# Kernel optimization log

Hardware: AMD Instinct MI355X
Metric: run time of the kernel (lower is better)

The kernel has to match this reference:

```python
import jax, jax.numpy as jnp
import numpy as np

B = 8
NF = 64
COUNTS = [1200, 1400, 1500, 1536, 1600, 1700, 1800, 1552]  # ragged per-batch point counts
ND = 12288  # total decoder points (= sum(COUNTS))
NE = 12288  # total encoder points
LQ = 1800   # max per-batch count (padding length)
EPS = 1e-4  # scn BatchNormalization eps


def _build_geometry():
    """Random sparse 3D voxel coords per batch on a 64^3 grid; parent cells (coord//2)
    are unique by construction so the stride-2 downsample keeps one point per cell
    and Nkv == Nd with the same per-batch ordering (matches the module's slicing)."""
    rng = np.random.default_rng(0)
    coords = []
    for b, c in enumerate(COUNTS):
        cells = rng.choice(32 * 32 * 32, size=c, replace=False)
        x, y, z = cells // 1024, (cells // 32) % 32, cells % 32
        off = rng.integers(0, 2, size=(c, 3))
        pts = np.stack([x, y, z], 1) * 2 + off
        coords.append(np.concatenate([np.full((c, 1), b), pts], 1))
    coords = np.concatenate(coords, 0)  # [ND, 4] = (batch, x, y, z)
    lut = {tuple(r): i for i, r in enumerate(coords)}
    offs = np.array([[dx, dy, dz] for dx in (-1, 0, 1) for dy in (-1, 0, 1) for dz in (-1, 0, 1)])
    nbr = np.full((ND, 27), -1, np.int32)  # 3^3 submanifold rulebook
    for i, r in enumerate(coords):
        for k, o in enumerate(offs):
            j = lut.get((r[0], r[1] + o[0], r[2] + o[1], r[3] + o[2]))
            if j is not None:
                nbr[i, k] = j
    kv_nbr = np.full((ND, 8), -1, np.int32)  # stride-2 2^3 conv rulebook (1 child per cell)
    off_id = (coords[:, 1] % 2) * 4 + (coords[:, 2] % 2) * 2 + (coords[:, 3] % 2)
    kv_nbr[np.arange(ND), off_id] = np.arange(ND)
    pad_idx = np.full((B, LQ), -1, np.int32)
    unpad_idx = np.zeros(ND, np.int32)
    s = 0
    for b, c in enumerate(COUNTS):
        pad_idx[b, :c] = np.arange(s, s + c)
        unpad_idx[s:s + c] = b * LQ + np.arange(c)
        s += c
    return nbr, kv_nbr, pad_idx, unpad_idx


def setup_inputs() -> dict:
    nbr, kv_nbr, pad_idx, unpad_idx = _build_geometry()
    key = jax.random.key(0)
    ks = jax.random.split(key, 16)
    w = lambda k, i, o: jax.random.normal(k, (i, o), jnp.float32) / np.sqrt(i)
    w3 = lambda k, t, i, o: jax.random.normal(k, (t, i, o), jnp.float32) / np.sqrt(t * i)
    return {
        "x_decoder": jax.random.normal(ks[0], (ND, NF), jnp.float32),
        "x_encoder": jax.random.normal(ks[1], (NE, NF), jnp.float32),
        "Wp1": w(ks[2], NF, NF), "Wq": w(ks[3], NF, NF), "Wk": w(ks[4], NF, NF),
        "Wv": w(ks[5], NF, NF), "Wt": w(ks[6], NF, NF), "Wq1": w(ks[7], NF, NF),
        "Wk1": w(ks[8], NF, NF), "Wv1": w(ks[9], NF, NF),
        "Wdown": w3(ks[10], 8, NF, NF),
        "W3t": w3(ks[11], 27, NF, NF), "W3a": w3(ks[12], 27, NF, NF), "W3b": w3(ks[13], 27, NF, NF),
        "bn_gamma": jnp.ones((6, NF), jnp.float32),
        "bn_beta": jnp.zeros((6, NF), jnp.float32),
        "nbr": jnp.asarray(nbr), "kv_nbr": jnp.asarray(kv_nbr),
        "pad_idx": jnp.asarray(pad_idx), "unpad_idx": jnp.asarray(unpad_idx),
    }


def _bn(x, g, b):  # training-mode scn.BatchNormalization over all active points
    m = jnp.mean(x, 0)
    v = jnp.mean(jnp.square(x - m), 0)
    return (x - m) * jax.lax.rsqrt(v + EPS) * g + b


def _gconv(f, idx, W):  # rulebook sparse conv: idx [N,K] (-1 = missing), W [K,F,O]
    mask = (idx >= 0).astype(f.dtype)[..., None]
    g = f[jnp.clip(idx, 0)] * mask  # [N, K, F]
    return jnp.einsum('nkf,kfo->no', g, W)


def _pad(f, pad_idx):  # flat [N,F] -> padded [B,L,F] + validity mask [B,L]
    m = pad_idx >= 0
    return f[jnp.clip(pad_idx, 0)] * m[..., None].astype(f.dtype), m


def reference(x_decoder, x_encoder, Wp1, Wq, Wk, Wv, Wt, Wq1, Wk1, Wv1,
              Wdown, W3t, W3a, W3b, bn_gamma, bn_beta,
              nbr, kv_nbr, pad_idx, unpad_idx):
    xd = x_decoder @ Wp1                      # p1 (1x1 submanifold conv)
    q = xd @ Wq
    ke = x_encoder @ Wk
    ve = x_encoder @ Wv
    # Stage-1 cross attention. The torch loop slices queries per batch but always
    # uses the FULL encoder K/V (dk = features.T), so it equals one global attention.
    attn = jax.nn.softmax(q @ ke.T, axis=-1)  # [ND, NE], no 1/sqrt(d) scaling in source
    xr = (attn @ ve) @ Wt                     # trans_conv (1x1)
    xd = xd + _bn(xr, bn_gamma[0], bn_beta[0])  # after_norm residual add

    q1 = xd @ Wq1
    kv = _bn(_gconv(q1, kv_nbr, Wdown), bn_gamma[1], bn_beta[1])  # stride-2 conv + BN
    k1 = kv @ Wk1
    v1 = kv @ Wv1
    # Stage-2 ragged per-batch self attention (Nkv == Nd by construction).
    qp, _ = _pad(q1, pad_idx)                 # [B, LQ, NF]
    kp, mkv = _pad(k1, pad_idx)
    vp, _ = _pad(v1, pad_idx)
    s2 = jnp.einsum('blf,bmf->blm', qp, kp)
    s2 = jnp.where(mkv[:, None, :], s2, jnp.float32(-1e30))
    o = jnp.einsum('blm,bmf->blf', jax.nn.softmax(s2, axis=-1), vp)
    xr2 = o.reshape(B * LQ, NF)[unpad_idx]    # back to flat ragged layout [ND, NF]
    xr2 = _gconv(xr2, nbr, W3t)               # trans_conv1 (3^3 submanifold conv)
    xd = xd + _bn(xr2, bn_gamma[2], bn_beta[2])  # after_norm1 residual add

    # res block: BNReLU -> conv3 -> BNReLU -> conv3, add identity, BNReLU
    z = _gconv(jax.nn.relu(_bn(xd, bn_gamma[3], bn_beta[3])), nbr, W3a)
    z = _gconv(jax.nn.relu(_bn(z, bn_gamma[4], bn_beta[4])), nbr, W3b)
    return jax.nn.relu(_bn(xd + z, bn_gamma[5], bn_beta[5]))
```

## Files before the change

### kernel.cpp

```cpp
#include <hip/hip_runtime.h>

#define NPTS 12288
#define LQPAD 1800
#define LPAD2 1856
#define EPSBN 1e-4f

typedef _Float16 half8 __attribute__((ext_vector_type(8)));
typedef _Float16 half4 __attribute__((ext_vector_type(4)));
typedef float floatx4 __attribute__((ext_vector_type(4)));

__global__ __launch_bounds__(256) void wprod(const float* __restrict__ Wp1, const float* __restrict__ Wq,
                                             float* __restrict__ Wpq) {
    __shared__ float A[4096], Bs[4096];
    int t = threadIdx.x;
    for (int i = t; i < 4096; i += 256) {
        A[i] = Wp1[i];
        Bs[i] = Wq[i];
    }
    __syncthreads();
    for (int o = 0; o < 16; o++) {
        int idx = o * 256 + t;
        int i = idx >> 6, j = idx & 63;
        float s = 0.f;
#pragma unroll
        for (int k = 0; k < 64; k++) s += A[i * 64 + k] * Bs[k * 64 + j];
        Wpq[idx] = s;
    }
}

__global__ __launch_bounds__(256) void pack_all(const float* Wp1, const float* Wpq, const float* Wk,
                                                const float* Wv, const float* Wt_, const float* Wq1,
                                                const float* Wk1, const float* Wv1, const float* Wdown,
                                                const float* W3t, const float* W3a, const float* W3b,
                                                _Float16* __restrict__ Wf) {
    int g = blockIdx.x;
    const float* src;
    if (g == 0) src = Wp1;
    else if (g == 1) src = Wpq;
    else if (g == 2) src = Wk;
    else if (g == 3) src = Wv;
    else if (g == 4) src = Wt_;
    else if (g == 5) src = Wq1;
    else if (g == 6) src = Wk1;
    else if (g == 7) src = Wv1;
    else if (g < 16) src = Wdown + (size_t)(g - 8) * 4096;
    else if (g < 43) src = W3t + (size_t)(g - 16) * 4096;
    else if (g < 70) src = W3a + (size_t)(g - 43) * 4096;
    else src = W3b + (size_t)(g - 70) * 4096;
    int t = threadIdx.x;
    int lane = t & 63, fg = t >> 6;
    int quad = lane >> 4, qi = lane & 15;
#pragma unroll
    for (int u = 0; u < 2; u++) {
        int frag = fg * 2 + u;
        int s = frag >> 2, ct = frag & 3;
        half8 v;
#pragma unroll
        for (int j = 0; j < 8; j++) v[j] = (_Float16)src[(s * 32 + quad * 8 + j) * 64 + ct * 16 + qi];
        *(half8*)(Wf + (size_t)g * 4096 + frag * 512 + lane * 8) = v;
    }
}

__device__ inline void load_split8(const float* p, half8& hi, half8& lo) {
    float4 a = *(const float4*)p;
    float4 b = *(const float4*)(p + 4);
    float v[8] = {a.x, a.y, a.z, a.w, b.x, b.y, b.z, b.w};
#pragma unroll
    for (int j = 0; j < 8; j++) {
        _Float16 h = (_Float16)v[j];
        hi[j] = h;
        lo[j] = (_Float16)(v[j] - (float)h);
    }
}

__global__ __launch_bounds__(256) void gemm_head(const float* __restrict__ xdec, const float* __restrict__ xenc,
                                                 const _Float16* __restrict__ Wf, float* __restrict__ xd,
                                                 _Float16* __restrict__ Qh, _Float16* __restrict__ Ql,
                                                 _Float16* __restrict__ Kh, _Float16* __restrict__ Vt) {
    int z = blockIdx.y;
    const float* A = (z < 2) ? xdec : xenc;
    const _Float16* Bf = Wf + (size_t)z * 4096;
    int t = threadIdx.x;
    int lane = t & 63, wv = t >> 6;
    int quad = lane >> 4, qi = lane & 15;
    int row0w = blockIdx.x * 64 + wv * 16;
    half8 ah[2], al[2];
#pragma unroll
    for (int s = 0; s < 2; s++) load_split8(A + (size_t)(row0w + qi) * 64 + s * 32 + quad * 8, ah[s], al[s]);
    floatx4 C[4];
#pragma unroll
    for (int ct = 0; ct < 4; ct++) C[ct] = floatx4{0.f, 0.f, 0.f, 0.f};
#pragma unroll
    for (int ct = 0; ct < 4; ct++)
#pragma unroll
        for (int s = 0; s < 2; s++) {
            half8 b = *(const half8*)(Bf + (s * 4 + ct) * 512 + lane * 8);
            C[ct] = __builtin_amdgcn_mfma_f32_16x16x32_f16(ah[s], b, C[ct], 0, 0, 0);
            C[ct] = __builtin_amdgcn_mfma_f32_16x16x32_f16(al[s], b, C[ct], 0, 0, 0);
        }
    int orow = row0w + quad * 4;
    if (z == 0) {
#pragma unroll
        for (int ct = 0; ct < 4; ct++)
#pragma unroll
            for (int r = 0; r < 4; r++) xd[(size_t)(orow + r) * 64 + ct * 16 + qi] = C[ct][r];
    } else if (z == 1) {
#pragma unroll
        for (int ct = 0; ct < 4; ct++)
#pragma unroll
            for (int r = 0; r < 4; r++) {
                float v = C[ct][r];
                _Float16 h = (_Float16)v;
                Qh[(size_t)(orow + r) * 64 + ct * 16 + qi] = h;
                Ql[(size_t)(orow + r) * 64 + ct * 16 + qi] = (_Float16)(v - (float)h);
            }
    } else if (z == 2) {
#pragma unroll
        for (int ct = 0; ct < 4; ct++)
#pragma unroll
            for (int r = 0; r < 4; r++) Kh[(size_t)(orow + r) * 64 + ct * 16 + qi] = (_Float16)C[ct][r];
    } else {
#pragma unroll
        for (int ct = 0; ct < 4; ct++) {
            half4 o;
#pragma unroll
            for (int r = 0; r < 4; r++) o[r] = (_Float16)C[ct][r];
            *(half4*)(Vt + (size_t)(ct * 16 + qi) * NPTS + orow) = o;
        }
    }
}

__global__ __launch_bounds__(256) void gemm_split(const float* __restrict__ A, const _Float16* __restrict__ Bf,
                                                  _Float16* __restrict__ Oh, _Float16* __restrict__ Ol) {
    int t = threadIdx.x;
    int lane = t & 63, wv = t >> 6;
    int quad = lane >> 4, qi = lane & 15;
    int row0w = blockIdx.x * 64 + wv * 16;
    half8 ah[2], al[2];
#pragma unroll
    for (int s = 0; s < 2; s++) load_split8(A + (size_t)(row0w + qi) * 64 + s * 32 + quad * 8, ah[s], al[s]);
    floatx4 C[4];
#pragma unroll
    for (int ct = 0; ct < 4; ct++) C[ct] = floatx4{0.f, 0.f, 0.f, 0.f};
#pragma unroll
    for (int ct = 0; ct < 4; ct++)
#pragma unroll
        for (int s = 0; s < 2; s++) {
            half8 b = *(const half8*)(Bf + (s * 4 + ct) * 512 + lane * 8);
            C[ct] = __builtin_amdgcn_mfma_f32_16x16x32_f16(ah[s], b, C[ct], 0, 0, 0);
            C[ct] = __builtin_amdgcn_mfma_f32_16x16x32_f16(al[s], b, C[ct], 0, 0, 0);
        }
    int orow = row0w + quad * 4;
#pragma unroll
    for (int ct = 0; ct < 4; ct++)
#pragma unroll
        for (int r = 0; r < 4; r++) {
            float v = C[ct][r];
            _Float16 h = (_Float16)v;
            Oh[(size_t)(orow + r) * 64 + ct * 16 + qi] = h;
            Ol[(size_t)(orow + r) * 64 + ct * 16 + qi] = (_Float16)(v - (float)h);
        }
}

__global__ __launch_bounds__(256) void gemm_kv1(const float* __restrict__ kv, const _Float16* __restrict__ Wfk,
                                                const _Float16* __restrict__ Wfv,
                                                const float* __restrict__ stats, const float* __restrict__ gamma,
                                                const float* __restrict__ beta, const int* __restrict__ unpad,
                                                _Float16* __restrict__ Kh1, _Float16* __restrict__ Vt2) {
    int y = blockIdx.y;
    int t = threadIdx.x;
    int lane = t & 63, wv = t >> 6;
    int quad = lane >> 4, qi = lane & 15;
    int row0w = blockIdx.x * 64 + wv * 16;
    const float inv_n = 1.f / (float)NPTS;
    half8 ah[2], al[2];
#pragma unroll
    for (int s = 0; s < 2; s++) {
        const float* p = kv + (size_t)(row0w + qi) * 64 + s * 32 + quad * 8;
        float4 a = *(const float4*)p;
        float4 b2 = *(const float4*)(p + 4);
        float v[8] = {a.x, a.y, a.z, a.w, b2.x, b2.y, b2.z, b2.w};
#pragma unroll
        for (int j = 0; j < 8; j++) {
            int f = s * 32 + quad * 8 + j;
            float mean = stats[f] * inv_n;
            float var = stats[64 + f] * inv_n - mean * mean;
            float val = (v[j] - mean) * rsqrtf(var + EPSBN) * gamma[f] + beta[f];
            _Float16 h = (_Float16)val;
            ah[s][j] = h;
            al[s][j] = (_Float16)(val - (float)h);
        }
    }
    const _Float16* Bf = y ? Wfv : Wfk;
    floatx4 C[4];
#pragma unroll
    for (int ct = 0; ct < 4; ct++) C[ct] = floatx4{0.f, 0.f, 0.f, 0.f};
#pragma unroll
    for (int ct = 0; ct < 4; ct++)
#pragma unroll
        for (int s = 0; s < 2; s++) {
            half8 b = *(const half8*)(Bf + (s * 4 + ct) * 512 + lane * 8);
            C[ct] = __builtin_amdgcn_mfma_f32_16x16x32_f16(ah[s], b, C[ct], 0, 0, 0);
            C[ct] = __builtin_amdgcn_mfma_f32_16x16x32_f16(al[s], b, C[ct], 0, 0, 0);
        }
    int orow = row0w + quad * 4;
    if (y == 0) {
#pragma unroll
        for (int ct = 0; ct < 4; ct++)
#pragma unroll
            for (int r = 0; r < 4; r++) Kh1[(size_t)(orow + r) * 64 + ct * 16 + qi] = (_Float16)C[ct][r];
    } else {
        int u0 = unpad[orow], u3 = unpad[orow + 3];
        int b0 = u0 / 1800, b3 = u3 / 1800;
        if (u3 == u0 + 3 && b0 == b3) {
            int p0 = u0 - b0 * 1800;
#pragma unroll
            for (int ct = 0; ct < 4; ct++) {
                half4 o;
#pragma unroll
                for (int r = 0; r < 4; r++) o[r] = (_Float16)C[ct][r];
                *(half4*)(Vt2 + ((size_t)b0 * 64 + ct * 16 + qi) * LPAD2 + p0) = o;
            }
        } else {
#pragma unroll
            for (int r = 0; r < 4; r++) {
                int u = unpad[orow + r];
                int b = u / 1800, p = u - b * 1800;
#pragma unroll
                for (int ct = 0; ct < 4; ct++)
                    Vt2[((size_t)b * 64 + ct * 16 + qi) * LPAD2 + p] = (_Float16)C[ct][r];
            }
        }
    }
}

__global__ __launch_bounds__(256) void gconv_mfma(const _Float16* __restrict__ Xh,
                                                  const int* __restrict__ idx,
                                                  const _Float16* __restrict__ Wf,
                                                  float* __restrict__ OUT, int nk,
                                                  const float* Xadd, float* stats_out) {
    __shared__ float s_sum[64], s_ss[64];
    int t = threadIdx.x;
    int lane = t & 63, wv = t >> 6;
    int quad = lane >> 4, qi = lane & 15;
    int row0 = blockIdx.x * 64 + wv * 16;
    if (stats_out) {
        if (t < 64) {
            s_sum[t] = 0.f;
            s_ss[t] = 0.f;
        }
        __syncthreads();
    }
    floatx4 Oacc[4];
#pragma unroll
    for (int ct = 0; ct < 4; ct++) Oacc[ct] = floatx4{0.f, 0.f, 0.f, 0.f};
    const int* ip = idx + (size_t)(row0 + qi) * nk;
    for (int k = 0; k < nk; k++) {
        int j = ip[k];
        half8 a0 = half8{0, 0, 0, 0, 0, 0, 0, 0};
        half8 a1 = half8{0, 0, 0, 0, 0, 0, 0, 0};
        if (j >= 0) {
            a0 = *(const half8*)(Xh + (size_t)j * 64 + quad * 8);
            a1 = *(const half8*)(Xh + (size_t)j * 64 + 32 + quad * 8);
        }
        const _Float16* wk = Wf + (size_t)k * 4096;
#pragma unroll
        for (int ct = 0; ct < 4; ct++) {
            half8 b0 = *(const half8*)(wk + ct * 512 + lane * 8);
            half8 b1 = *(const half8*)(wk + (4 + ct) * 512 + lane * 8);
            Oacc[ct] = __builtin_amdgcn_mfma_f32_16x16x32_f16(a0, b0, Oacc[ct], 0, 0, 0);
            Oacc[ct] = __builtin_amdgcn_mfma_f32_16x16x32_f16(a1, b1, Oacc[ct], 0, 0, 0);
        }
    }
    int orow = row0 + quad * 4;
#pragma unroll
    for (int ct = 0; ct < 4; ct++)
#pragma unroll
        for (int r = 0; r < 4; r++) OUT[(size_t)(orow + r) * 64 + ct * 16 + qi] = Oacc[ct][r];
    if (stats_out) {
#pragma unroll
        for (int ct = 0; ct < 4; ct++) {
            int f = ct * 16 + qi;
            float ps = 0.f, pss = 0.f;
#pragma unroll
            for (int r = 0; r < 4; r++) {
                float v = Oacc[ct][r];
                if (Xadd) v += Xadd[(size_t)(orow + r) * 64 + f];
                ps += v;
                pss += v * v;
            }
            atomicAdd(&s_sum[f], ps);
            atomicAdd(&s_ss[f], pss);
        }
        __syncthreads();
        if (t < 64) {
            atomicAdd(&stats_out[t], s_sum[t]);
            atomicAdd(&stats_out[64 + t], s_ss[t]);
        }
    }
}

__global__ __launch_bounds__(256) void bn_apply(const float* __restrict__ X, const float* X2,
                                                const float* R, float* OUT, _Float16* OUT16,
                                                const float* __restrict__ stats,
                                                const float* __restrict__ gamma,
                                                const float* __restrict__ beta,
                                                float* stats_out, int n, int do_relu) {
    __shared__ float sh[2][4][64];
    int t = threadIdx.x;
    int f = t & 63, g = t >> 6;
    float inv_n = 1.f / (float)n;
    float mean = stats[f] * inv_n;
    float var = stats[64 + f] * inv_n - mean * mean;
    float rstd = rsqrtf(var + EPSBN);
    float ga = gamma[f], be = beta[f];
    float s = 0.f, ss = 0.f;
    for (int r = blockIdx.x * 4 + g; r < n; r += gridDim.x * 4) {
        size_t i = (size_t)r * 64 + f;
        float v = X[i];
        if (X2) v += X2[i];
        v = (v - mean) * rstd * ga + be;
        if (R) v += R[i];
        if (do_relu) v = fmaxf(v, 0.f);
        if (OUT) OUT[i] = v;
        if (OUT16) OUT16[i] = (_Float16)v;
        s += v;
        ss += v * v;
    }
    if (stats_out) {
        sh[0][g][f] = s;
        sh[1][g][f] = ss;
        __syncthreads();
        if (g == 0) {
            s = sh[0][0][f] + sh[0][1][f] + sh[0][2][f] + sh[0][3][f];
            ss = sh[1][0][f] + sh[1][1][f] + sh[1][2][f] + sh[1][3][f];
            atomicAdd(&stats_out[f], s);
            atomicAdd(&stats_out[64 + f], ss);
        }
    }
}

__global__ __launch_bounds__(256) void count_valid(const int* __restrict__ pad_idx, int* __restrict__ counts) {
    int b = blockIdx.x;
    int t = threadIdx.x;
    int s = 0;
    for (int i = t; i < LQPAD; i += 256) s += (pad_idx[b * LQPAD + i] >= 0) ? 1 : 0;
    for (int off = 32; off > 0; off >>= 1) s += __shfl_xor(s, off);
    if ((t & 63) == 0) atomicAdd(&counts[b], s);
}

__global__ __launch_bounds__(256, 3) void flash1_mfma(const _Float16* __restrict__ Qh,
                                                      const _Float16* __restrict__ Ql,
                                                      const _Float16* __restrict__ Kh,
                                                      const _Float16* __restrict__ Vt,
                                                      _Float16* __restrict__ Op,
                                                      float* __restrict__ Ms,
                                                      float* __restrict__ Ls) {
    __shared__ __align__(16) _Float16 KsF[8 * 512];
    __shared__ __align__(16) _Float16 VsF[8 * 512];
    __shared__ __align__(16) _Float16 PTF[4][2 * 1024];
    int t = threadIdx.x;
    int lane = t & 63, wv = t >> 6;
    int quad = lane >> 4, qi = lane & 15;
    int qb = blockIdx.x, sp = blockIdx.y;
    int q0w = qb * 128 + wv * 32;

    half8 qh[2][2], ql[2][2];
#pragma unroll
    for (int sub = 0; sub < 2; sub++)
#pragma unroll
        for (int s = 0; s < 2; s++) {
            int qrow = q0w + sub * 16 + qi;
            qh[sub][s] = *(const half8*)(Qh + (size_t)qrow * 64 + s * 32 + quad * 8);
            ql[sub][s] = *(const half8*)(Ql + (size_t)qrow * 64 + s * 32 + quad * 8);
        }
    floatx4 Oacc[2][4];
#pragma unroll
    for (int sub = 0; sub < 2; sub++)
#pragma unroll
        for (int ft = 0; ft < 4; ft++) Oacc[sub][ft] = floatx4{0.f, 0.f, 0.f, 0.f};
    float m_i[2] = {-1e30f, -1e30f}, l_i[2] = {0.f, 0.f};

    for (int it = 0; it < 24; it++) {
        int k0 = sp * 1536 + it * 64;
        __syncthreads();
#pragma unroll
        for (int u = 0; u < 4; u++) {
            int frag = wv + 4 * u;
            if (frag < 8) {
                int kt = frag >> 1, s = frag & 1;
                int key = k0 + kt * 16 + qi;
                *(half8*)(KsF + frag * 512 + lane * 8) =
                    *(const half8*)(Kh + (size_t)key * 64 + s * 32 + quad * 8);
            } else {
                int fr = frag - 8;
                int ft = fr >> 1, s = fr & 1;
                int f = ft * 16 + qi;
                *(half8*)(VsF + fr * 512 + lane * 8) =
                    *(const half8*)(Vt + (size_t)f * NPTS + k0 + s * 32 + quad * 8);
            }
        }
        __syncthreads();
        half8 ka[4][2];
#pragma unroll
        for (int kt = 0; kt < 4; kt++)
#pragma unroll
            for (int s = 0; s < 2; s++) ka[kt][s] = *(const half8*)(KsF + (kt * 2 + s) * 512 + lane * 8);
        floatx4 st[2][4];
#pragma unroll
        for (int sub = 0; sub < 2; sub++)
#pragma unroll
            for (int kt = 0; kt < 4; kt++) {
                floatx4 acc = floatx4{0.f, 0.f, 0.f, 0.f};
#pragma unroll
                for (int s = 0; s < 2; s++) {
                    acc = __builtin_amdgcn_mfma_f32_16x16x32_f16(ka[kt][s], qh[sub][s], acc, 0, 0, 0);
                    acc = __builtin_amdgcn_mfma_f32_16x16x32_f16(ka[kt][s], ql[sub][s], acc, 0, 0, 0);
                }
                st[sub][kt] = acc;
            }
#pragma unroll
        for (int sub = 0; sub < 2; sub++) {
            float mloc = -1e30f;
#pragma unroll
            for (int kt = 0; kt < 4; kt++)
#pragma unroll
                for (int r = 0; r < 4; r++) mloc = fmaxf(mloc, st[sub][kt][r]);
            mloc = fmaxf(mloc, __shfl_xor(mloc, 16));
            mloc = fmaxf(mloc, __shfl_xor(mloc, 32));
            float m_new = fmaxf(m_i[sub], mloc);
            float alpha = __expf(m_i[sub] - m_new);
            float ps = 0.f;
#pragma unroll
            for (int kt = 0; kt < 4; kt++) {
                half4 pk;
#pragma unroll
                for (int r = 0; r < 4; r++) {
                    float p = __expf(st[sub][kt][r] - m_new);
                    ps += p;
                    pk[r] = (_Float16)p;
                }
                int s = kt >> 1;
                int qd2 = (kt & 1) * 2 + (quad >> 1);
                *(half4*)(&PTF[wv][sub * 1024 + (s * 64 + qd2 * 16 + qi) * 8 + (quad & 1) * 4]) = pk;
            }
            ps += __shfl_xor(ps, 16);
            ps += __shfl_xor(ps, 32);
            l_i[sub] = l_i[sub] * alpha + ps;
            m_i[sub] = m_new;
#pragma unroll
            for (int ft = 0; ft < 4; ft++) Oacc[sub][ft] *= alpha;
        }
        half8 pb[2][2];
#pragma unroll
        for (int sub = 0; sub < 2; sub++)
#pragma unroll
            for (int s = 0; s < 2; s++)
                pb[sub][s] = *(const half8*)(&PTF[wv][sub * 1024 + (s * 64 + lane) * 8]);
#pragma unroll
        for (int ft = 0; ft < 4; ft++)
#pragma unroll
            for (int s = 0; s < 2; s++) {
                half8 v = *(const half8*)(VsF + (ft * 2 + s) * 512 + lane * 8);
                Oacc[0][ft] = __builtin_amdgcn_mfma_f32_16x16x32_f16(v, pb[0][s], Oacc[0][ft], 0, 0, 0);
                Oacc[1][ft] = __builtin_amdgcn_mfma_f32_16x16x32_f16(v, pb[1][s], Oacc[1][ft], 0, 0, 0);
            }
    }
#pragma unroll
    for (int sub = 0; sub < 2; sub++) {
#pragma unroll
        for (int ft = 0; ft < 4; ft++) {
            half4 o;
#pragma unroll
            for (int r = 0; r < 4; r++) o[r] = (_Float16)Oacc[sub][ft][r];
            *(half4*)(Op + ((size_t)sp * NPTS + q0w + sub * 16 + qi) * 64 + ft * 16 + quad * 4) = o;
        }
        if (lane < 16) {
            Ms[sp * NPTS + q0w + sub * 16 + lane] = m_i[sub];
            Ls[sp * NPTS + q0w + sub * 16 + lane] = l_i[sub];
        }
    }
}

__global__ __launch_bounds__(256) void merge_gemm(const _Float16* __restrict__ Op,
                                                  const float* __restrict__ Ms, const float* __restrict__ Ls,
                                                  const _Float16* __restrict__ Wtf,
                                                  float* __restrict__ xr, float* __restrict__ stats_out) {
    __shared__ float w8[64][8];
    __shared__ float Linv[64];
    __shared__ __align__(16) _Float16 Ah[64 * 72], Al[64 * 72];
    __shared__ float s_sum[64], s_ss[64];
    int t = threadIdx.x;
    int row0 = blockIdx.x * 64;
    if (t < 64) {
        int q = row0 + t;
        float m[8], M = -1e30f;
#pragma unroll
        for (int s = 0; s < 8; s++) {
            m[s] = Ms[s * NPTS + q];
            M = fmaxf(M, m[s]);
        }
        float L = 0.f;
#pragma unroll
        for (int s = 0; s < 8; s++) {
            float w = __expf(m[s] - M);
            w8[t][s] = w;
            L += Ls[s * NPTS + q] * w;
        }
        Linv[t] = 1.f / L;
        s_sum[t] = 0.f;
        s_ss[t] = 0.f;
    }
    __syncthreads();
    for (int k = 0; k < 4; k++) {
        int i = t + k * 256;
        int qr = i >> 4, f4 = (i & 15) * 4;
        int q = row0 + qr;
        float acc[4] = {0.f, 0.f, 0.f, 0.f};
#pragma unroll
        for (int s = 0; s < 8; s++) {
            float w = w8[qr][s];
            half4 o = *(const half4*)(Op + ((size_t)s * NPTS + q) * 64 + f4);
#pragma unroll
            for (int c = 0; c < 4; c++) acc[c] += (float)o[c] * w;
        }
        float inv = Linv[qr];
#pragma unroll
        for (int c = 0; c < 4; c++) {
            float val = acc[c] * inv;
            _Float16 h = (_Float16)val;
            Ah[qr * 72 + f4 + c] = h;
            Al[qr * 72 + f4 + c] = (_Float16)(val - (float)h);
        }
    }
    __syncthreads();
    int lane = t & 63, wv = t >> 6;
    int quad = lane >> 4, qi = lane & 15;
    int rloc = wv * 16 + qi;
    half8 ah[2], al[2];
#pragma unroll
    for (int s = 0; s < 2; s++) {
        ah[s] = *(const half8*)(Ah + rloc * 72 + s * 32 + quad * 8);
        al[s] = *(const half8*)(Al + rloc * 72 + s * 32 + quad * 8);
    }
    floatx4 C[4];
#pragma unroll
    for (int ct = 0; ct < 4; ct++) C[ct] = floatx4{0.f, 0.f, 0.f, 0.f};
#pragma unroll
    for (int ct = 0; ct < 4; ct++)
#pragma unroll
        for (int s = 0; s < 2; s++) {
            half8 b = *(const half8*)(Wtf + (s * 4 + ct) * 512 + lane * 8);
            C[ct] = __builtin_amdgcn_mfma_f32_16x16x32_f16(ah[s], b, C[ct], 0, 0, 0);
            C[ct] = __builtin_amdgcn_mfma_f32_16x16x32_f16(al[s], b, C[ct], 0, 0, 0);
        }
    int orow = row0 + wv * 16 + quad * 4;
#pragma unroll
    for (int ct = 0; ct < 4; ct++) {
        int f = ct * 16 + qi;
        float ps = 0.f, pss = 0.f;
#pragma unroll
        for (int r = 0; r < 4; r++) {
            float v = C[ct][r];
            xr[(size_t)(orow + r) * 64 + f] = v;
            ps += v;
            pss += v * v;
        }
        atomicAdd(&s_sum[f], ps);
        atomicAdd(&s_ss[f], pss);
    }
    __syncthreads();
    if (t < 64) {
        atomicAdd(&stats_out[t], s_sum[t]);
        atomicAdd(&stats_out[64 + t], s_ss[t]);
    }
}

__global__ __launch_bounds__(256) void flash2_mfma(const _Float16* __restrict__ Qh,
                                                   const _Float16* __restrict__ Ql,
                                                   const _Float16* __restrict__ Kh,
                                                   const _Float16* __restrict__ Vt2,
                                                   const int* __restrict__ pad_idx,
                                                   const int* __restrict__ counts,
                                                   _Float16* __restrict__ O) {
    int b = blockIdx.y;
    int c = counts[b];
    int qb = blockIdx.x;
    if (qb * 64 >= c) return;
    __shared__ __align__(16) _Float16 KsF[8 * 512];
    __shared__ __align__(16) _Float16 VsF[8 * 512];
    __shared__ __align__(16) _Float16 PTF[4][2 * 512];
    int t = threadIdx.x;
    int lane = t & 63, wv = t >> 6;
    int quad = lane >> 4, qi = lane & 15;
    const int* prow = pad_idx + b * LQPAD;
    int p_q = qb * 64 + wv * 16 + qi;
    int flat_q = (p_q < LQPAD) ? prow[p_q] : -1;

    half8 qh[2], ql[2];
#pragma unroll
    for (int s = 0; s < 2; s++) {
        if (flat_q >= 0) {
            qh[s] = *(const half8*)(Qh + (size_t)flat_q * 64 + s * 32 + quad * 8);
            ql[s] = *(const half8*)(Ql + (size_t)flat_q * 64 + s * 32 + quad * 8);
        } else {
            qh[s] = half8{0, 0, 0, 0, 0, 0, 0, 0};
            ql[s] = half8{0, 0, 0, 0, 0, 0, 0, 0};
        }
    }
    floatx4 Oacc[4];
#pragma unroll
    for (int ft = 0; ft < 4; ft++) Oacc[ft] = floatx4{0.f, 0.f, 0.f, 0.f};
    float m_i = -1e30f, l_i = 0.f;
    const _Float16* VtB = Vt2 + (size_t)b * 64 * LPAD2;

    int nt = (c + 63) >> 6;
    for (int it = 0; it < nt; it++) {
        int k0 = it * 64;
        __syncthreads();
#pragma unroll
        for (int u = 0; u < 4; u++) {
            int frag = wv + 4 * u;
            if (frag < 8) {
                int kt = frag >> 1, s = frag & 1;
                int kp = k0 + kt * 16 + qi;
                int flat = (kp < c) ? prow[kp] : -1;
                int d0 = s * 32 + quad * 8;
                half8 kvv = half8{0, 0, 0, 0, 0, 0, 0, 0};
                if (flat >= 0) kvv = *(const half8*)(Kh + (size_t)flat * 64 + d0);
                *(half8*)(KsF + frag * 512 + lane * 8) = kvv;
            } else {
                int fr = frag - 8;
                int ft = fr >> 1, s = fr & 1;
                int f = ft * 16 + qi;
                int key = k0 + s * 32 + quad * 8;
                *(half8*)(VsF + fr * 512 + lane * 8) = *(const half8*)(VtB + f * LPAD2 + key);
            }
        }
        __syncthreads();
        floatx4 st[4];
#pragma unroll
        for (int kt = 0; kt < 4; kt++) {
            floatx4 acc = floatx4{0.f, 0.f, 0.f, 0.f};
#pragma unroll
            for (int s = 0; s < 2; s++) {
                half8 a = *(const half8*)(KsF + (kt * 2 + s) * 512 + lane * 8);
                acc = __builtin_amdgcn_mfma_f32_16x16x32_f16(a, qh[s], acc, 0, 0, 0);
                acc = __builtin_amdgcn_mfma_f32_16x16x32_f16(a, ql[s], acc, 0, 0, 0);
            }
            st[kt] = acc;
        }
        float mloc = -1e30f;
#pragma unroll
        for (int kt = 0; kt < 4; kt++)
#pragma unroll
            for (int r = 0; r < 4; r++) mloc = fmaxf(mloc, st[kt][r]);
        mloc = fmaxf(mloc, __shfl_xor(mloc, 16));
        mloc = fmaxf(mloc, __shfl_xor(mloc, 32));
        float m_new = fmaxf(m_i, mloc);
        float alpha = __expf(m_i - m_new);
        float ps = 0.f;
#pragma unroll
        for (int kt = 0; kt < 4; kt++) {
            half4 pk;
#pragma unroll
            for (int r = 0; r < 4; r++) {
                int kpos = k0 + kt * 16 + quad * 4 + r;
                float p = (kpos < c) ? __expf(st[kt][r] - m_new) : 0.f;
                ps += p;
                pk[r] = (_Float16)p;
            }
            int s = kt >> 1;
            int qd2 = (kt & 1) * 2 + (quad >> 1);
            *(half4*)(&PTF[wv][(s * 64 + qd2 * 16 + qi) * 8 + (quad & 1) * 4]) = pk;
        }
        ps += __shfl_xor(ps, 16);
        ps += __shfl_xor(ps, 32);
        l_i = l_i * alpha + ps;
        m_i = m_new;
#pragma unroll
        for (int ft = 0; ft < 4; ft++) Oacc[ft] *= alpha;
        half8 pb[2];
#pragma unroll
        for (int s = 0; s < 2; s++) pb[s] = *(const half8*)(&PTF[wv][(s * 64 + lane) * 8]);
#pragma unroll
        for (int ft = 0; ft < 4; ft++)
#pragma unroll
            for (int s = 0; s < 2; s++) {
                half8 a = *(const half8*)(VsF + (ft * 2 + s) * 512 + lane * 8);
                Oacc[ft] = __builtin_amdgcn_mfma_f32_16x16x32_f16(a, pb[s], Oacc[ft], 0, 0, 0);
            }
    }
    if (flat_q >= 0) {
        float inv = 1.f / l_i;
#pragma unroll
        for (int ft = 0; ft < 4; ft++) {
            half4 o;
#pragma unroll
            for (int r = 0; r < 4; r++) o[r] = (_Float16)(Oacc[ft][r] * inv);
            *(half4*)(O + (size_t)flat_q * 64 + ft * 16 + quad * 4) = o;
        }
    }
}

extern "C" void kernel_launch(void* const* d_in, const int* in_sizes, int n_in,
                              void* d_out, int out_size, void* d_ws, size_t ws_size,
                              hipStream_t stream) {
    const float* x_dec = (const float*)d_in[0];
    const float* x_enc = (const float*)d_in[1];
    const float* Wp1 = (const float*)d_in[2];
    const float* Wq = (const float*)d_in[3];
    const float* Wk = (const float*)d_in[4];
    const float* Wv = (const float*)d_in[5];
    const float* Wt_ = (const float*)d_in[6];
    const float* Wq1 = (const float*)d_in[7];
    const float* Wk1 = (const float*)d_in[8];
    const float* Wv1 = (const float*)d_in[9];
    const float* Wdown = (const float*)d_in[10];
    const float* W3t = (const float*)d_in[11];
    const float* W3a = (const float*)d_in[12];
    const float* W3b = (const float*)d_in[13];
    const float* bn_g = (const float*)d_in[14];
    const float* bn_b = (const float*)d_in[15];
    const int* nbr = (const int*)d_in[16];
    const int* kv_nbr = (const int*)d_in[17];
    const int* pad_idx = (const int*)d_in[18];
    const int* unpad_idx = (const int*)d_in[19];
    float* out = (float*)d_out;
    float* ws = (float*)d_ws;

    const int N = NPTS;
    const size_t BUF = (size_t)N * 64;
    float* xd = ws;
    float* slot1 = ws + BUF;
    float* slot2 = ws + 2 * BUF;
    float* slot3 = ws + 3 * BUF;
    float* slot4 = ws + 4 * BUF;
    float* slot5 = ws + 5 * BUF;
    float* slot6 = ws + 6 * BUF;
    float* slot7 = ws + 7 * BUF;
    float* slot8 = ws + 8 * BUF;
    float* arena = ws + 9 * BUF;

    float* stats = arena;
    int* counts = (int*)(arena + 768);
    float* Ms = arena + 1024;
    float* Ls = Ms + 8 * NPTS;
    _Float16* WfA = (_Float16*)(Ls + 8 * NPTS);
    float* Wpq = (float*)(WfA + (size_t)97 * 4096);

    _Float16* Oph = (_Float16*)slot1;
    _Float16* Qh = (_Float16*)slot5;
    _Float16* Ql = Qh + BUF;
    _Float16* Kh = (_Float16*)slot6;
    _Float16* Vt = Kh + BUF;
    float* kv = slot5;
    _Float16* Qh1 = (_Float16*)slot2;
    _Float16* Ql1 = Qh1 + BUF;
    _Float16* Kh1 = (_Float16*)slot6;
    _Float16* Vt2 = (_Float16*)slot1;
    _Float16* z2h = (_Float16*)slot4;
    float* xr = slot7;
    _Float16* xrh = (_Float16*)slot7;
    float* xr2 = slot8;
    float* o2 = slot8;
    _Float16* xr2h = (_Float16*)slot6;
    float* z2 = slot3;

    const _Float16* Wp1f = WfA;
    const _Float16* Wpqf = WfA + 1 * 4096;
    const _Float16* Wtf = WfA + 4 * 4096;
    const _Float16* Wq1f = WfA + 5 * 4096;
    const _Float16* Wk1f = WfA + 6 * 4096;
    const _Float16* Wv1f = WfA + 7 * 4096;
    const _Float16* Wdf = WfA + 8 * 4096;
    const _Float16* W3tf = WfA + (size_t)16 * 4096;
    const _Float16* W3af = WfA + (size_t)43 * 4096;
    const _Float16* W3bf = WfA + (size_t)70 * 4096;
    (void)Wp1f;

    hipMemsetAsync(stats, 0, 1024 * sizeof(float), stream);

    dim3 B(256);
    int gG = N / 64;

    wprod<<<1, B, 0, stream>>>(Wp1, Wq, Wpq);
    pack_all<<<97, B, 0, stream>>>(Wp1, Wpq, Wk, Wv, Wt_, Wq1, Wk1, Wv1, Wdown, W3t, W3a, W3b, WfA);
    count_valid<<<8, B, 0, stream>>>(pad_idx, counts);

    gemm_head<<<dim3(gG, 4), B, 0, stream>>>(x_dec, x_enc, WfA, xd, Qh, Ql, Kh, Vt);
    flash1_mfma<<<dim3(N / 128, 8), B, 0, stream>>>(Qh, Ql, Kh, Vt, Oph, Ms, Ls);
    merge_gemm<<<gG, B, 0, stream>>>(Oph, Ms, Ls, Wtf, xr, stats + 0);
    bn_apply<<<256, B, 0, stream>>>(xr, nullptr, xd, xd, nullptr, stats + 0, bn_g + 0, bn_b + 0,
                                    nullptr, N, 0);

    gemm_split<<<gG, B, 0, stream>>>(xd, Wq1f, Qh1, Ql1);
    gconv_mfma<<<gG, B, 0, stream>>>(Qh1, kv_nbr, Wdf, kv, 8, nullptr, stats + 128);
    gemm_kv1<<<dim3(gG, 2), B, 0, stream>>>(kv, Wk1f, Wv1f, stats + 128, bn_g + 64, bn_b + 64,
                                            unpad_idx, Kh1, Vt2);
    flash2_mfma<<<dim3(LPAD2 / 64, 8), B, 0, stream>>>(Qh1, Ql1, Kh1, Vt2, pad_idx, counts, z2h);
    gconv_mfma<<<gG, B, 0, stream>>>(z2h, nbr, W3tf, xr2, 27, nullptr, stats + 256);
    bn_apply<<<256, B, 0, stream>>>(xr2, nullptr, xd, xd, nullptr, stats + 256, bn_g + 128, bn_b + 128,
                                    stats + 384, N, 0);

    bn_apply<<<256, B, 0, stream>>>(xd, nullptr, nullptr, nullptr, xrh, stats + 384, bn_g + 192,
                                    bn_b + 192, nullptr, N, 1);
    gconv_mfma<<<gG, B, 0, stream>>>(xrh, nbr, W3af, o2, 27, nullptr, stats + 512);
    bn_apply<<<256, B, 0, stream>>>(o2, nullptr, nullptr, nullptr, xr2h, stats + 512, bn_g + 256,
                                    bn_b + 256, nullptr, N, 1);
    gconv_mfma<<<gG, B, 0, stream>>>(xr2h, nbr, W3bf, z2, 27, xd, stats + 640);
    bn_apply<<<256, B, 0, stream>>>(xd, z2, nullptr, out, nullptr, stats + 640, bn_g + 320, bn_b + 320,
                                    nullptr, N, 1);
}
```

Measured before the change: 433.6 us.

## Parallelize wprod, fuse BN into q1 GEMM, split gconv columns, widen flash1 key tile

New measurement: 415.2 us. 1.04x faster.

```diff
diff --git a/kernel.cpp b/kernel.cpp
--- a/kernel.cpp
+++ b/kernel.cpp
@@ -9,23 +9,23 @@
 typedef _Float16 half4 __attribute__((ext_vector_type(4)));
 typedef float floatx4 __attribute__((ext_vector_type(4)));
 
-__global__ __launch_bounds__(256) void wprod(const float* __restrict__ Wp1, const float* __restrict__ Wq,
-                                             float* __restrict__ Wpq) {
-    __shared__ float A[4096], Bs[4096];
-    int t = threadIdx.x;
-    for (int i = t; i < 4096; i += 256) {
-        A[i] = Wp1[i];
-        Bs[i] = Wq[i];
+__global__ __launch_bounds__(256) void wprod16(const float* __restrict__ Wp1, const float* __restrict__ Wq,
+                                               float* __restrict__ Wpq) {
+    __shared__ float Bs[4096];
+    __shared__ float As[4][64];
+    int t = threadIdx.x;
+    for (int i = t; i < 4096; i += 256) Bs[i] = Wq[i];
+    int r0 = blockIdx.x * 4;
+    {
+        int i = t >> 6, k = t & 63;
+        As[i][k] = Wp1[(r0 + i) * 64 + k];
     }
     __syncthreads();
-    for (int o = 0; o < 16; o++) {
-        int idx = o * 256 + t;
-        int i = idx >> 6, j = idx & 63;
-        float s = 0.f;
-#pragma unroll
-        for (int k = 0; k < 64; k++) s += A[i * 64 + k] * Bs[k * 64 + j];
-        Wpq[idx] = s;
-    }
+    int i = t >> 6, j = t & 63;
+    float s = 0.f;
+#pragma unroll
+    for (int k = 0; k < 64; k++) s += As[i][k] * Bs[k * 64 + j];
+    Wpq[(r0 + i) * 64 + j] = s;
 }
 
 __global__ __launch_bounds__(256) void pack_all(const float* Wp1, const float* Wpq, const float* Wk,
@@ -130,15 +130,42 @@
     }
 }
 
-__global__ __launch_bounds__(256) void gemm_split(const float* __restrict__ A, const _Float16* __restrict__ Bf,
-                                                  _Float16* __restrict__ Oh, _Float16* __restrict__ Ol) {
+__global__ __launch_bounds__(256) void gemm_q1(const float* __restrict__ xr, float* __restrict__ xd,
+                                               const _Float16* __restrict__ Bf,
+                                               const float* __restrict__ stats,
+                                               const float* __restrict__ gamma,
+                                               const float* __restrict__ beta,
+                                               _Float16* __restrict__ Oh, _Float16* __restrict__ Ol) {
     int t = threadIdx.x;
     int lane = t & 63, wv = t >> 6;
     int quad = lane >> 4, qi = lane & 15;
     int row0w = blockIdx.x * 64 + wv * 16;
+    const float inv_n = 1.f / (float)NPTS;
     half8 ah[2], al[2];
 #pragma unroll
-    for (int s = 0; s < 2; s++) load_split8(A + (size_t)(row0w + qi) * 64 + s * 32 + quad * 8, ah[s], al[s]);
+    for (int s = 0; s < 2; s++) {
+        size_t base = (size_t)(row0w + qi) * 64 + s * 32 + quad * 8;
+        float4 xa = *(const float4*)(xr + base);
+        float4 xb = *(const float4*)(xr + base + 4);
+        float4 da = *(const float4*)(xd + base);
+        float4 db = *(const float4*)(xd + base + 4);
+        float vx[8] = {xa.x, xa.y, xa.z, xa.w, xb.x, xb.y, xb.z, xb.w};
+        float vd[8] = {da.x, da.y, da.z, da.w, db.x, db.y, db.z, db.w};
+        float vo[8];
+#pragma unroll
+        for (int j = 0; j < 8; j++) {
+            int f = s * 32 + quad * 8 + j;
+            float mean = stats[f] * inv_n;
+            float var = stats[64 + f] * inv_n - mean * mean;
+            float val = vd[j] + (vx[j] - mean) * rsqrtf(var + EPSBN) * gamma[f] + beta[f];
+            vo[j] = val;
+            _Float16 h = (_Float16)val;
+            ah[s][j] = h;
+            al[s][j] = (_Float16)(val - (float)h);
+        }
+        *(float4*)(xd + base) = float4{vo[0], vo[1], vo[2], vo[3]};
+        *(float4*)(xd + base + 4) = float4{vo[4], vo[5], vo[6], vo[7]};
+    }
     floatx4 C[4];
 #pragma unroll
     for (int ct = 0; ct < 4; ct++) C[ct] = floatx4{0.f, 0.f, 0.f, 0.f};
@@ -243,7 +270,9 @@
     int t = threadIdx.x;
     int lane = t & 63, wv = t >> 6;
     int quad = lane >> 4, qi = lane & 15;
-    int row0 = blockIdx.x * 64 + wv * 16;
+    int bx = blockIdx.x;
+    int row0 = (bx >> 1) * 64 + wv * 16;
+    int cb = (bx & 1) * 2;
     if (stats_out) {
         if (t < 64) {
             s_sum[t] = 0.f;
@@ -251,9 +280,9 @@
         }
         __syncthreads();
     }
-    floatx4 Oacc[4];
-#pragma unroll
-    for (int ct = 0; ct < 4; ct++) Oacc[ct] = floatx4{0.f, 0.f, 0.f, 0.f};
+    floatx4 Oacc[2];
+#pragma unroll
+    for (int u = 0; u < 2; u++) Oacc[u] = floatx4{0.f, 0.f, 0.f, 0.f};
     const int* ip = idx + (size_t)(row0 + qi) * nk;
     for (int k = 0; k < nk; k++) {
         int j = ip[k];
@@ -265,26 +294,29 @@
         }
         const _Float16* wk = Wf + (size_t)k * 4096;
 #pragma unroll
-        for (int ct = 0; ct < 4; ct++) {
+        for (int u = 0; u < 2; u++) {
+            int ct = cb + u;
             half8 b0 = *(const half8*)(wk + ct * 512 + lane * 8);
             half8 b1 = *(const half8*)(wk + (4 + ct) * 512 + lane * 8);
-            Oacc[ct] = __builtin_amdgcn_mfma_f32_16x16x32_f16(a0, b0, Oacc[ct], 0, 0, 0);
-            Oacc[ct] = __builtin_amdgcn_mfma_f32_16x16x32_f16(a1, b1, Oacc[ct], 0, 0, 0);
+            Oacc[u] = __builtin_amdgcn_mfma_f32_16x16x32_f16(a0, b0, Oacc[u], 0, 0, 0);
+            Oacc[u] = __builtin_amdgcn_mfma_f32_16x16x32_f16(a1, b1, Oacc[u], 0, 0, 0);
         }
     }
     int orow = row0 + quad * 4;
 #pragma unroll
-    for (int ct = 0; ct < 4; ct++)
-#pragma unroll
-        for (int r = 0; r < 4; r++) OUT[(size_t)(orow + r) * 64 + ct * 16 + qi] = Oacc[ct][r];
+    for (int u = 0; u < 2; u++) {
+        int ct = cb + u;
+#pragma unroll
+        for (int r = 0; r < 4; r++) OUT[(size_t)(orow + r) * 64 + ct * 16 + qi] = Oacc[u][r];
+    }
     if (stats_out) {
 #pragma unroll
-        for (int ct = 0; ct < 4; ct++) {
-            int f = ct * 16 + qi;
+        for (int u = 0; u < 2; u++) {
+            int f = (cb + u) * 16 + qi;
             float ps = 0.f, pss = 0.f;
 #pragma unroll
             for (int r = 0; r < 4; r++) {
-                float v = Oacc[ct][r];
+                float v = Oacc[u][r];
                 if (Xadd) v += Xadd[(size_t)(orow + r) * 64 + f];
                 ps += v;
                 pss += v * v;
@@ -356,8 +388,8 @@
                                                       _Float16* __restrict__ Op,
                                                       float* __restrict__ Ms,
                                                       float* __restrict__ Ls) {
-    __shared__ __align__(16) _Float16 KsF[8 * 512];
-    __shared__ __align__(16) _Float16 VsF[8 * 512];
+    __shared__ __align__(16) _Float16 KsF[16 * 512];
+    __shared__ __align__(16) _Float16 VsF[16 * 512];
     __shared__ __align__(16) _Float16 PTF[4][2 * 1024];
     int t = threadIdx.x;
     int lane = t & 63, wv = t >> 6;
@@ -381,90 +413,94 @@
         for (int ft = 0; ft < 4; ft++) Oacc[sub][ft] = floatx4{0.f, 0.f, 0.f, 0.f};
     float m_i[2] = {-1e30f, -1e30f}, l_i[2] = {0.f, 0.f};
 
-    for (int it = 0; it < 24; it++) {
-        int k0 = sp * 1536 + it * 64;
+    for (int it = 0; it < 12; it++) {
+        int k0 = sp * 1536 + it * 128;
         __syncthreads();
 #pragma unroll
-        for (int u = 0; u < 4; u++) {
+        for (int u = 0; u < 8; u++) {
             int frag = wv + 4 * u;
-            if (frag < 8) {
+            if (frag < 16) {
                 int kt = frag >> 1, s = frag & 1;
                 int key = k0 + kt * 16 + qi;
                 *(half8*)(KsF + frag * 512 + lane * 8) =
                     *(const half8*)(Kh + (size_t)key * 64 + s * 32 + quad * 8);
             } else {
-                int fr = frag - 8;
-                int ft = fr >> 1, s = fr & 1;
+                int fr = frag - 16;
+                int ft = fr >> 2, s = fr & 3;
                 int f = ft * 16 + qi;
                 *(half8*)(VsF + fr * 512 + lane * 8) =
                     *(const half8*)(Vt + (size_t)f * NPTS + k0 + s * 32 + quad * 8);
             }
         }
         __syncthreads();
-        half8 ka[4][2];
-#pragma unroll
-        for (int kt = 0; kt < 4; kt++)
-#pragma unroll
-            for (int s = 0; s < 2; s++) ka[kt][s] = *(const half8*)(KsF + (kt * 2 + s) * 512 + lane * 8);
-        floatx4 st[2][4];
-#pragma unroll
-        for (int sub = 0; sub < 2; sub++)
-#pragma unroll
-            for (int kt = 0; kt < 4; kt++) {
-                floatx4 acc = floatx4{0.f, 0.f, 0.f, 0.f};
+#pragma unroll
+        for (int ch = 0; ch < 2; ch++) {
+            half8 ka[4][2];
+#pragma unroll
+            for (int kt = 0; kt < 4; kt++)
+#pragma unroll
+                for (int s = 0; s < 2; s++)
+                    ka[kt][s] = *(const half8*)(KsF + ((ch * 4 + kt) * 2 + s) * 512 + lane * 8);
+            floatx4 st[2][4];
+#pragma unroll
+            for (int sub = 0; sub < 2; sub++)
+#pragma unroll
+                for (int kt = 0; kt < 4; kt++) {
+                    floatx4 acc = floatx4{0.f, 0.f, 0.f, 0.f};
+#pragma unroll
+                    for (int s = 0; s < 2; s++) {
+                        acc = __builtin_amdgcn_mfma_f32_16x16x32_f16(ka[kt][s], qh[sub][s], acc, 0, 0, 0);
+                        acc = __builtin_amdgcn_mfma_f32_16x16x32_f16(ka[kt][s], ql[sub][s], acc, 0, 0, 0);
+                    }
+                    st[sub][kt] = acc;
+                }
+#pragma unroll
+            for (int sub = 0; sub < 2; sub++) {
+                float mloc = -1e30f;
+#pragma unroll
+                for (int kt = 0; kt < 4; kt++)
+#pragma unroll
+                    for (int r = 0; r < 4; r++) mloc = fmaxf(mloc, st[sub][kt][r]);
+                mloc = fmaxf(mloc, __shfl_xor(mloc, 16));
+                mloc = fmaxf(mloc, __shfl_xor(mloc, 32));
+                float m_new = fmaxf(m_i[sub], mloc);
+                float alpha = __expf(m_i[sub] - m_new);
+                float ps = 0.f;
+#pragma unroll
+                for (int kt = 0; kt < 4; kt++) {
+                    half4 pk;
+#pragma unroll
+                    for (int r = 0; r < 4; r++) {
+                        float p = __expf(st[sub][kt][r] - m_new);
+                        ps += p;
+                        pk[r] = (_Float16)p;
+                    }
+                    int s = kt >> 1;
+                    int qd2 = (kt & 1) * 2 + (quad >> 1);
+                    *(half4*)(&PTF[wv][sub * 1024 + (s * 64 + qd2 * 16 + qi) * 8 + (quad & 1) * 4]) = pk;
+                }
+                ps += __shfl_xor(ps, 16);
+                ps += __shfl_xor(ps, 32);
+                l_i[sub] = l_i[sub] * alpha + ps;
+                m_i[sub] = m_new;
+#pragma unroll
+                for (int ft = 0; ft < 4; ft++) Oacc[sub][ft] *= alpha;
+            }
+            half8 pb[2][2];
+#pragma unroll
+            for (int sub = 0; sub < 2; sub++)
+#pragma unroll
+                for (int s = 0; s < 2; s++)
+                    pb[sub][s] = *(const half8*)(&PTF[wv][sub * 1024 + (s * 64 + lane) * 8]);
+#pragma unroll
+            for (int ft = 0; ft < 4; ft++)
 #pragma unroll
                 for (int s = 0; s < 2; s++) {
-                    acc = __builtin_amdgcn_mfma_f32_16x16x32_f16(ka[kt][s], qh[sub][s], acc, 0, 0, 0);
-                    acc = __builtin_amdgcn_mfma_f32_16x16x32_f16(ka[kt][s], ql[sub][s], acc, 0, 0, 0);
+                    half8 v = *(const half8*)(VsF + (ft * 4 + ch * 2 + s) * 512 + lane * 8);
+                    Oacc[0][ft] = __builtin_amdgcn_mfma_f32_16x16x32_f16(v, pb[0][s], Oacc[0][ft], 0, 0, 0);
+                    Oacc[1][ft] = __builtin_amdgcn_mfma_f32_16x16x32_f16(v, pb[1][s], Oacc[1][ft], 0, 0, 0);
                 }
-                st[sub][kt] = acc;
-            }
-#pragma unroll
-        for (int sub = 0; sub < 2; sub++) {
-            float mloc = -1e30f;
-#pragma unroll
-            for (int kt = 0; kt < 4; kt++)
-#pragma unroll
-                for (int r = 0; r < 4; r++) mloc = fmaxf(mloc, st[sub][kt][r]);
-            mloc = fmaxf(mloc, __shfl_xor(mloc, 16));
-            mloc = fmaxf(mloc, __shfl_xor(mloc, 32));
-            float m_new = fmaxf(m_i[sub], mloc);
-            float alpha = __expf(m_i[sub] - m_new);
-            float ps = 0.f;
-#pragma unroll
-            for (int kt = 0; kt < 4; kt++) {
-                half4 pk;
-#pragma unroll
-                for (int r = 0; r < 4; r++) {
-                    float p = __expf(st[sub][kt][r] - m_new);
-                    ps += p;
-                    pk[r] = (_Float16)p;
-                }
-                int s = kt >> 1;
-                int qd2 = (kt & 1) * 2 + (quad >> 1);
-                *(half4*)(&PTF[wv][sub * 1024 + (s * 64 + qd2 * 16 + qi) * 8 + (quad & 1) * 4]) = pk;
-            }
-            ps += __shfl_xor(ps, 16);
-            ps += __shfl_xor(ps, 32);
-            l_i[sub] = l_i[sub] * alpha + ps;
-            m_i[sub] = m_new;
-#pragma unroll
-            for (int ft = 0; ft < 4; ft++) Oacc[sub][ft] *= alpha;
-        }
-        half8 pb[2][2];
-#pragma unroll
-        for (int sub = 0; sub < 2; sub++)
-#pragma unroll
-            for (int s = 0; s < 2; s++)
-                pb[sub][s] = *(const half8*)(&PTF[wv][sub * 1024 + (s * 64 + lane) * 8]);
-#pragma unroll
-        for (int ft = 0; ft < 4; ft++)
-#pragma unroll
-            for (int s = 0; s < 2; s++) {
-                half8 v = *(const half8*)(VsF + (ft * 2 + s) * 512 + lane * 8);
-                Oacc[0][ft] = __builtin_amdgcn_mfma_f32_16x16x32_f16(v, pb[0][s], Oacc[0][ft], 0, 0, 0);
-                Oacc[1][ft] = __builtin_amdgcn_mfma_f32_16x16x32_f16(v, pb[1][s], Oacc[1][ft], 0, 0, 0);
-            }
+        }
     }
 #pragma unroll
     for (int sub = 0; sub < 2; sub++) {
@@ -767,8 +803,6 @@
     _Float16* xr2h = (_Float16*)slot6;
     float* z2 = slot3;
 
-    const _Float16* Wp1f = WfA;
-    const _Float16* Wpqf = WfA + 1 * 4096;
     const _Float16* Wtf = WfA + 4 * 4096;
     const _Float16* Wq1f = WfA + 5 * 4096;
     const _Float16* Wk1f = WfA + 6 * 4096;
@@ -777,38 +811,36 @@
     const _Float16* W3tf = WfA + (size_t)16 * 4096;
     const _Float16* W3af = WfA + (size_t)43 * 4096;
     const _Float16* W3bf = WfA + (size_t)70 * 4096;
-    (void)Wp1f;
 
     hipMemsetAsync(stats, 0, 1024 * sizeof(float), stream);
 
     dim3 B(256);
     int gG = N / 64;
-
-    wprod<<<1, B, 0, stream>>>(Wp1, Wq, Wpq);
+    int gC2 = 2 * gG;
+
+    wprod16<<<16, B, 0, stream>>>(Wp1, Wq, Wpq);
     pack_all<<<97, B, 0, stream>>>(Wp1, Wpq, Wk, Wv, Wt_, Wq1, Wk1, Wv1, Wdown, W3t, W3a, W3b, WfA);
     count_valid<<<8, B, 0, stream>>>(pad_idx, counts);
 
     gemm_head<<<dim3(gG, 4), B, 0, stream>>>(x_dec, x_enc, WfA, xd, Qh, Ql, Kh, Vt);
     flash1_mfma<<<dim3(N / 128, 8), B, 0, stream>>>(Qh, Ql, Kh, Vt, Oph, Ms, Ls);
     merge_gemm<<<gG, B, 0, stream>>>(Oph, Ms, Ls, Wtf, xr, stats + 0);
-    bn_apply<<<256, B, 0, stream>>>(xr, nullptr, xd, xd, nullptr, stats + 0, bn_g + 0, bn_b + 0,
-                                    nullptr, N, 0);
-
-    gemm_split<<<gG, B, 0, stream>>>(xd, Wq1f, Qh1, Ql1);
-    gconv_mfma<<<gG, B, 0, stream>>>(Qh1, kv_nbr, Wdf, kv, 8, nullptr, stats + 128);
+    gemm_q1<<<gG, B, 0, stream>>>(xr, xd, Wq1f, stats + 0, bn_g + 0, bn_b + 0, Qh1, Ql1);
+
+    gconv_mfma<<<gC2, B, 0, stream>>>(Qh1, kv_nbr, Wdf, kv, 8, nullptr, stats + 128);
     gemm_kv1<<<dim3(gG, 2), B, 0, stream>>>(kv, Wk1f, Wv1f, stats + 128, bn_g + 64, bn_b + 64,
                                             unpad_idx, Kh1, Vt2);
     flash2_mfma<<<dim3(LPAD2 / 64, 8), B, 0, stream>>>(Qh1, Ql1, Kh1, Vt2, pad_idx, counts, z2h);
-    gconv_mfma<<<gG, B, 0, stream>>>(z2h, nbr, W3tf, xr2, 27, nullptr, stats + 256);
+    gconv_mfma<<<gC2, B, 0, stream>>>(z2h, nbr, W3tf, xr2, 27, nullptr, stats + 256);
     bn_apply<<<256, B, 0, stream>>>(xr2, nullptr, xd, xd, nullptr, stats + 256, bn_g + 128, bn_b + 128,
                                     stats + 384, N, 0);
 
     bn_apply<<<256, B, 0, stream>>>(xd, nullptr, nullptr, nullptr, xrh, stats + 384, bn_g + 192,
                                     bn_b + 192, nullptr, N, 1);
-    gconv_mfma<<<gG, B, 0, stream>>>(xrh, nbr, W3af, o2, 27, nullptr, stats + 512);
+    gconv_mfma<<<gC2, B, 0, stream>>>(xrh, nbr, W3af, o2, 27, nullptr, stats + 512);
     bn_apply<<<256, B, 0, stream>>>(o2, nullptr, nullptr, nullptr, xr2h, stats + 512, bn_g + 256,
                                     bn_b + 256, nullptr, N, 1);
-    gconv_mfma<<<gG, B, 0, stream>>>(xr2h, nbr, W3bf, z2, 27, xd, stats + 640);
+    gconv_mfma<<<gC2, B, 0, stream>>>(xr2h, nbr, W3bf, z2, 27, xd, stats + 640);
     bn_apply<<<256, B, 0, stream>>>(xd, z2, nullptr, out, nullptr, stats + 640, bn_g + 320, bn_b + 320,
                                     nullptr, N, 1);
 }
```
